# Kernel tuning notes

Hardware: AMD Instinct MI355X
Metric: run time of the kernel (lower is better)

## Reference

```python
import jax, jax.numpy as jnp
import numpy as np

N_NODES = 100000
N_EDGES = 1600000
IN_DIM = 64
HID_DIM = 32


def setup_inputs() -> dict:
    key = jax.random.key(0)
    k1, k2, k3, k4 = jax.random.split(key, 4)
    features = jax.random.normal(k1, (N_NODES, IN_DIM), dtype=jnp.float32)
    src = jax.random.randint(k2, (N_EDGES,), 0, N_NODES, dtype=jnp.int32)
    dst = jax.random.randint(k3, (N_EDGES,), 0, N_NODES, dtype=jnp.int32)
    # Glorot-uniform weight as in DGL GraphConv reset_parameters
    limit = (6.0 / (IN_DIM + HID_DIM)) ** 0.5
    W = jax.random.uniform(k4, (IN_DIM, HID_DIM), dtype=jnp.float32,
                           minval=-limit, maxval=limit)
    b = jnp.zeros((HID_DIM,), dtype=jnp.float32)
    return {"features": features, "src": src, "dst": dst, "W": W, "b": b}


def reference(features, src, dst, W, b):
    """DGL GraphConv(norm='both', activation=relu):
    out = relu(D_in^{-1/2} A D_out^{-1/2} (X W) + b)
    (weight applied first since in_dim > out_dim)."""
    n = features.shape[0]
    ones = jnp.ones(src.shape[0], dtype=features.dtype)
    deg_out = jax.ops.segment_sum(ones, src, num_segments=n)  # out-degree
    deg_in = jax.ops.segment_sum(ones, dst, num_segments=n)   # in-degree
    norm_src = jnp.clip(deg_out, 1.0, None) ** -0.5          # [N]
    norm_dst = jnp.clip(deg_in, 1.0, None) ** -0.5           # [N]

    h = (features @ W) * norm_src[:, None]                    # [N, hid]
    msg = h[src]                                              # [E, hid] gather
    agg = jax.ops.segment_sum(msg, dst, num_segments=n)       # [N, hid] scatter-add
    out = agg * norm_dst[:, None] + b
    return jax.nn.relu(out)
```

## Files before the change

### kernel.cpp

```cpp
#include <hip/hip_runtime.h>
#include <hip/hip_fp16.h>

#define IN_DIM 64
#define HID 32
#define SHIFT 8
#define BKEYS 256
#define CAP 4608
#define HCAP 2560
#define CHUNK 4096
#define MAXB 512

__global__ void zero_kernel(unsigned* __restrict__ p) {
    p[threadIdx.x + blockIdx.x * 256] = 0u;
}

__global__ __launch_bounds__(512) void multisplit_kernel(
    const int* __restrict__ src, const int* __restrict__ dst, int E, int NB,
    unsigned* __restrict__ gcur_d, unsigned* __restrict__ gcur_s,
    unsigned* __restrict__ bkt_pairs, unsigned char* __restrict__ bkt_srcs)
{
    __shared__ unsigned hist_d[MAXB], cur_d[MAXB], gb_d[MAXB];
    __shared__ unsigned hist_s[MAXB], cur_s[MAXB], gb_s[MAXB];
    int t = threadIdx.x;
    int e0 = blockIdx.x * CHUNK;
    int cnt = min(CHUNK, E - e0);
    hist_d[t] = 0; hist_s[t] = 0; cur_d[t] = 0; cur_s[t] = 0;
    __syncthreads();
    int n4 = cnt >> 2;
    const int4* s4 = (const int4*)(src + e0);
    const int4* d4 = (const int4*)(dst + e0);
    int4 sa = make_int4(-1, -1, -1, -1), da = sa, sb = sa, db = sa;
    if (t < n4)       { sa = s4[t];       da = d4[t]; }
    if (t + 512 < n4) { sb = s4[t + 512]; db = d4[t + 512]; }
    int sc = -1, dc = -1;
    int ti = (n4 << 2) + t;
    if (t < (cnt & 3)) { sc = src[e0 + ti]; dc = dst[e0 + ti]; }
    if (da.x >= 0) { atomicAdd(&hist_d[da.x >> SHIFT], 1u); atomicAdd(&hist_s[sa.x >> SHIFT], 1u);
                     atomicAdd(&hist_d[da.y >> SHIFT], 1u); atomicAdd(&hist_s[sa.y >> SHIFT], 1u);
                     atomicAdd(&hist_d[da.z >> SHIFT], 1u); atomicAdd(&hist_s[sa.z >> SHIFT], 1u);
                     atomicAdd(&hist_d[da.w >> SHIFT], 1u); atomicAdd(&hist_s[sa.w >> SHIFT], 1u); }
    if (db.x >= 0) { atomicAdd(&hist_d[db.x >> SHIFT], 1u); atomicAdd(&hist_s[sb.x >> SHIFT], 1u);
                     atomicAdd(&hist_d[db.y >> SHIFT], 1u); atomicAdd(&hist_s[sb.y >> SHIFT], 1u);
                     atomicAdd(&hist_d[db.z >> SHIFT], 1u); atomicAdd(&hist_s[sb.z >> SHIFT], 1u);
                     atomicAdd(&hist_d[db.w >> SHIFT], 1u); atomicAdd(&hist_s[sb.w >> SHIFT], 1u); }
    if (dc >= 0)   { atomicAdd(&hist_d[dc >> SHIFT], 1u);   atomicAdd(&hist_s[sc >> SHIFT], 1u); }
    __syncthreads();
    if (t < NB) {
        unsigned hd = hist_d[t], hs = hist_s[t];
        if (hd) gb_d[t] = atomicAdd(&gcur_d[t], hd);
        if (hs) gb_s[t] = atomicAdd(&gcur_s[t], hs);
    }
    __syncthreads();
    int dv[9] = {da.x, da.y, da.z, da.w, db.x, db.y, db.z, db.w, dc};
    int sv[9] = {sa.x, sa.y, sa.z, sa.w, sb.x, sb.y, sb.z, sb.w, sc};
#pragma unroll
    for (int j = 0; j < 9; ++j) {
        if (dv[j] < 0) continue;
        int kd = dv[j] >> SHIFT;
        unsigned pos = gb_d[kd] + atomicAdd(&cur_d[kd], 1u);
        if (pos < CAP)
            bkt_pairs[(size_t)kd * CAP + pos] =
                (((unsigned)dv[j] & (BKEYS - 1)) << 17) | (unsigned)sv[j];
        int ks = sv[j] >> SHIFT;
        unsigned pos2 = gb_s[ks] + atomicAdd(&cur_s[ks], 1u);
        if (pos2 < CAP)
            bkt_srcs[(size_t)ks * CAP + pos2] = (unsigned char)(sv[j] & (BKEYS - 1));
    }
}

__global__ __launch_bounds__(512) void degxw_kernel(
    const unsigned char* __restrict__ bkt_srcs, const unsigned* __restrict__ gcur_s,
    const float* __restrict__ X, const float* __restrict__ W,
    int N, unsigned short* __restrict__ h16)
{
    __shared__ float Ws[IN_DIM * HID];
    __shared__ unsigned cnt[128];
    __shared__ float nrm[128];
    int t = threadIdx.x;
    int blk = blockIdx.x, bin = blk >> 1;
    unsigned half = blk & 1;
    ((float4*)Ws)[t] = ((const float4*)W)[t];
    if (t < 128) cnt[t] = 0;
    __syncthreads();
    unsigned m = gcur_s[bin];
    if (m > CAP) m = CAP;
    const unsigned char* bs = bkt_srcs + (size_t)bin * CAP;
    const uchar4* bs4 = (const uchar4*)bs;
    unsigned m4 = m >> 2;
    for (unsigned i = t; i < m4; i += 512) {
        uchar4 kk = bs4[i];
        if ((kk.x >> 7) == half) atomicAdd(&cnt[kk.x & 127], 1u);
        if ((kk.y >> 7) == half) atomicAdd(&cnt[kk.y & 127], 1u);
        if ((kk.z >> 7) == half) atomicAdd(&cnt[kk.z & 127], 1u);
        if ((kk.w >> 7) == half) atomicAdd(&cnt[kk.w & 127], 1u);
    }
    for (unsigned i = (m4 << 2) + t; i < m; i += 512) {
        unsigned k = bs[i];
        if ((k >> 7) == half) atomicAdd(&cnt[k & 127], 1u);
    }
    __syncthreads();
    if (t < 128) nrm[t] = rsqrtf(fmaxf((float)cnt[t], 1.0f));
    __syncthreads();
    int q = t & 7, ln = t >> 3;
#pragma unroll
    for (int pass = 0; pass < 2; ++pass) {
        int lv = pass * 64 + ln;
        int v = bin * BKEYS + (int)half * 128 + lv;
        if (v < N) {
            const float4* Xr = (const float4*)(X + (size_t)v * IN_DIM);
            float4 acc = make_float4(0.f, 0.f, 0.f, 0.f);
#pragma unroll
            for (int kk = 0; kk < 16; ++kk) {
                float4 xv = Xr[kk];
                int k0 = kk * 4;
                float4 w0 = ((float4*)Ws)[(k0 + 0) * 8 + q];
                float4 w1 = ((float4*)Ws)[(k0 + 1) * 8 + q];
                float4 w2 = ((float4*)Ws)[(k0 + 2) * 8 + q];
                float4 w3 = ((float4*)Ws)[(k0 + 3) * 8 + q];
                acc.x += xv.x * w0.x + xv.y * w1.x + xv.z * w2.x + xv.w * w3.x;
                acc.y += xv.x * w0.y + xv.y * w1.y + xv.z * w2.y + xv.w * w3.y;
                acc.z += xv.x * w0.z + xv.y * w1.z + xv.z * w2.z + xv.w * w3.z;
                acc.w += xv.x * w0.w + xv.y * w1.w + xv.z * w2.w + xv.w * w3.w;
            }
            float s = nrm[lv];
            __half2 a  = __floats2half2_rn(acc.x * s, acc.y * s);
            __half2 b2 = __floats2half2_rn(acc.z * s, acc.w * s);
            uint2 u;
            u.x = *(unsigned*)&a;
            u.y = *(unsigned*)&b2;
            ((uint2*)h16)[(size_t)v * 8 + q] = u;
        }
    }
}

__global__ __launch_bounds__(512) void csrgather_kernel(
    const unsigned* __restrict__ bkt_pairs, const unsigned* __restrict__ gcur_d,
    const unsigned short* __restrict__ h16, const float* __restrict__ bias,
    float* __restrict__ out, int N)
{
    __shared__ unsigned cnt[128], ex[128], cur[128];
    __shared__ unsigned ecsr[HCAP];
    int t = threadIdx.x;
    int blk = blockIdx.x, bin = blk >> 1;
    unsigned half = blk & 1;
    if (t < 128) { cnt[t] = 0; cur[t] = 0; }
    __syncthreads();
    unsigned m = gcur_d[bin];
    if (m > CAP) m = CAP;
    const unsigned* bp = bkt_pairs + (size_t)bin * CAP;
    for (unsigned i = t; i < m; i += 512) {
        unsigned k = bp[i] >> 17;
        if ((k >> 7) == half) atomicAdd(&cnt[k & 127], 1u);
    }
    __syncthreads();
    if (t < 128) ex[t] = cnt[t];
    __syncthreads();
    for (int off = 1; off < 128; off <<= 1) {
        unsigned u = (t >= off && t < 128) ? ex[t - off] : 0;
        __syncthreads();
        if (t < 128) ex[t] += u;
        __syncthreads();
    }
    for (unsigned i = t; i < m; i += 512) {
        unsigned p = bp[i];
        unsigned k = p >> 17;
        if ((k >> 7) == half) {
            unsigned kk = k & 127;
            unsigned pos = (ex[kk] - cnt[kk]) + atomicAdd(&cur[kk], 1u);
            if (pos < HCAP) ecsr[pos] = p & 0x1FFFFu;
        }
    }
    __syncthreads();
    int lane = t & 63, w = t >> 6;
    int n16 = lane >> 2;
    int q = lane & 3;
    int lv = w * 16 + n16;
    unsigned dg = cnt[lv];
    unsigned en = ex[lv]; if (en > HCAP) en = HCAP;
    unsigned st = ex[lv] - dg; if (st > en) st = en;
    unsigned len = en - st;
    const uint4* h16q = (const uint4*)h16;

    float a0=0.f,a1=0.f,a2=0.f,a3=0.f,a4=0.f,a5=0.f,a6=0.f,a7=0.f;
    unsigned i = 0;
    for (; i + 4 <= len; i += 4) {
        unsigned s0 = ecsr[st + i];
        unsigned s1 = ecsr[st + i + 1];
        unsigned s2 = ecsr[st + i + 2];
        unsigned s3 = ecsr[st + i + 3];
        uint4 h0 = h16q[(size_t)s0 * 4 + q];
        uint4 h1 = h16q[(size_t)s1 * 4 + q];
        uint4 h2 = h16q[(size_t)s2 * 4 + q];
        uint4 h3 = h16q[(size_t)s3 * 4 + q];
        __half2* p0 = (__half2*)&h0;  __half2* p1 = (__half2*)&h1;
        __half2* p2 = (__half2*)&h2;  __half2* p3 = (__half2*)&h3;
        float2 f;
        f = __half22float2(p0[0]); a0 += f.x; a1 += f.y;
        f = __half22float2(p0[1]); a2 += f.x; a3 += f.y;
        f = __half22float2(p0[2]); a4 += f.x; a5 += f.y;
        f = __half22float2(p0[3]); a6 += f.x; a7 += f.y;
        f = __half22float2(p1[0]); a0 += f.x; a1 += f.y;
        f = __half22float2(p1[1]); a2 += f.x; a3 += f.y;
        f = __half22float2(p1[2]); a4 += f.x; a5 += f.y;
        f = __half22float2(p1[3]); a6 += f.x; a7 += f.y;
        f = __half22float2(p2[0]); a0 += f.x; a1 += f.y;
        f = __half22float2(p2[1]); a2 += f.x; a3 += f.y;
        f = __half22float2(p2[2]); a4 += f.x; a5 += f.y;
        f = __half22float2(p2[3]); a6 += f.x; a7 += f.y;
        f = __half22float2(p3[0]); a0 += f.x; a1 += f.y;
        f = __half22float2(p3[1]); a2 += f.x; a3 += f.y;
        f = __half22float2(p3[2]); a4 += f.x; a5 += f.y;
        f = __half22float2(p3[3]); a6 += f.x; a7 += f.y;
    }
    for (; i < len; ++i) {
        unsigned s = ecsr[st + i];
        uint4 hv = h16q[(size_t)s * 4 + q];
        __half2* hp = (__half2*)&hv;
        float2 f;
        f = __half22float2(hp[0]); a0 += f.x; a1 += f.y;
        f = __half22float2(hp[1]); a2 += f.x; a3 += f.y;
        f = __half22float2(hp[2]); a4 += f.x; a5 += f.y;
        f = __half22float2(hp[3]); a6 += f.x; a7 += f.y;
    }
    int v = bin * BKEYS + (int)half * 128 + lv;
    if (v < N) {
        float nv = rsqrtf(fmaxf((float)dg, 1.0f));
        float4 bq0 = ((const float4*)bias)[q * 2];
        float4 bq1 = ((const float4*)bias)[q * 2 + 1];
        float4 o0, o1;
        o0.x = fmaxf(a0 * nv + bq0.x, 0.f);
        o0.y = fmaxf(a1 * nv + bq0.y, 0.f);
        o0.z = fmaxf(a2 * nv + bq0.z, 0.f);
        o0.w = fmaxf(a3 * nv + bq0.w, 0.f);
        o1.x = fmaxf(a4 * nv + bq1.x, 0.f);
        o1.y = fmaxf(a5 * nv + bq1.y, 0.f);
        o1.z = fmaxf(a6 * nv + bq1.z, 0.f);
        o1.w = fmaxf(a7 * nv + bq1.w, 0.f);
        float* op = out + (size_t)v * HID + q * 8;
        *(float4*)op = o0;
        *(float4*)(op + 4) = o1;
    }
}

extern "C" void kernel_launch(void* const* d_in, const int* in_sizes, int n_in,
                              void* d_out, int out_size, void* d_ws, size_t ws_size,
                              hipStream_t stream) {
    const float* X   = (const float*)d_in[0];
    const int*   src = (const int*)d_in[1];
    const int*   dst = (const int*)d_in[2];
    const float* W   = (const float*)d_in[3];
    const float* b   = (const float*)d_in[4];
    float* out = (float*)d_out;

    int N = in_sizes[0] / IN_DIM;
    int E = in_sizes[1];
    int NB = (N + BKEYS - 1) / BKEYS;

    unsigned* gcur_d = (unsigned*)d_ws;
    unsigned* gcur_s = gcur_d + MAXB;
    unsigned* bkt_pairs = gcur_s + MAXB;
    unsigned char* bkt_srcs = (unsigned char*)(bkt_pairs + (size_t)NB * CAP);
    unsigned short* h16 = (unsigned short*)(bkt_srcs + (size_t)NB * CAP);

    zero_kernel<<<4, 256, 0, stream>>>(gcur_d);
    multisplit_kernel<<<(E + CHUNK - 1) / CHUNK, 512, 0, stream>>>(
        src, dst, E, NB, gcur_d, gcur_s, bkt_pairs, bkt_srcs);
    degxw_kernel<<<NB * 2, 512, 0, stream>>>(bkt_srcs, gcur_s, X, W, N, h16);
    csrgather_kernel<<<NB * 2, 512, 0, stream>>>(bkt_pairs, gcur_d, h16, b, out, N);
}
```

Baseline: 145.9 us.

## Split fp16 hidden features into two column planes to shrink gather working set

The fp16 projected features are stored as two separate 16-column planes instead of one interleaved 32-column row. The gather kernel now launches twice as many 256-thread blocks, each handling one plane, so each block gathers 32-byte rows from a half-size table. The intent is better cache locality for the random source-row gathers, since each plane's table fits more easily in L2/MALL. The cost is that every block rebuilds the bucket CSR in shared memory, so the edge-bucket scan and scatter work is doubled.

New measurement: 155.7 us. 1.07x slower.

```diff
diff --git a/kernel.cpp b/kernel.cpp
--- a/kernel.cpp
+++ b/kernel.cpp
@@ -102,6 +102,8 @@
     if (t < 128) nrm[t] = rsqrtf(fmaxf((float)cnt[t], 1.0f));
     __syncthreads();
     int q = t & 7, ln = t >> 3;
+    int plane = q >> 2, jq = q & 3;
+    uint2* hp = (uint2*)h16 + (size_t)plane * N * 4;
 #pragma unroll
     for (int pass = 0; pass < 2; ++pass) {
         int lv = pass * 64 + ln;
@@ -128,27 +130,30 @@
             uint2 u;
             u.x = *(unsigned*)&a;
             u.y = *(unsigned*)&b2;
-            ((uint2*)h16)[(size_t)v * 8 + q] = u;
+            hp[(size_t)v * 4 + jq] = u;
         }
     }
 }
 
-__global__ __launch_bounds__(512) void csrgather_kernel(
+__global__ __launch_bounds__(256) void csrgather_kernel(
     const unsigned* __restrict__ bkt_pairs, const unsigned* __restrict__ gcur_d,
     const unsigned short* __restrict__ h16, const float* __restrict__ bias,
-    float* __restrict__ out, int N)
+    float* __restrict__ out, int N, int NB)
 {
     __shared__ unsigned cnt[128], ex[128], cur[128];
     __shared__ unsigned ecsr[HCAP];
     int t = threadIdx.x;
-    int blk = blockIdx.x, bin = blk >> 1;
-    unsigned half = blk & 1;
+    int blk = blockIdx.x;
+    int plane = (blk >= 2 * NB) ? 1 : 0;
+    int blk2 = blk - plane * 2 * NB;
+    int bin = blk2 >> 1;
+    unsigned half = blk2 & 1;
     if (t < 128) { cnt[t] = 0; cur[t] = 0; }
     __syncthreads();
     unsigned m = gcur_d[bin];
     if (m > CAP) m = CAP;
     const unsigned* bp = bkt_pairs + (size_t)bin * CAP;
-    for (unsigned i = t; i < m; i += 512) {
+    for (unsigned i = t; i < m; i += 256) {
         unsigned k = bp[i] >> 17;
         if ((k >> 7) == half) atomicAdd(&cnt[k & 127], 1u);
     }
@@ -161,7 +166,7 @@
         if (t < 128) ex[t] += u;
         __syncthreads();
     }
-    for (unsigned i = t; i < m; i += 512) {
+    for (unsigned i = t; i < m; i += 256) {
         unsigned p = bp[i];
         unsigned k = p >> 17;
         if ((k >> 7) == half) {
@@ -172,14 +177,14 @@
     }
     __syncthreads();
     int lane = t & 63, w = t >> 6;
-    int n16 = lane >> 2;
-    int q = lane & 3;
-    int lv = w * 16 + n16;
+    int n32 = lane >> 1;
+    int j = lane & 1;
+    int lv = w * 32 + n32;
     unsigned dg = cnt[lv];
     unsigned en = ex[lv]; if (en > HCAP) en = HCAP;
     unsigned st = ex[lv] - dg; if (st > en) st = en;
     unsigned len = en - st;
-    const uint4* h16q = (const uint4*)h16;
+    const uint4* hq = (const uint4*)h16 + (size_t)plane * N * 2;
 
     float a0=0.f,a1=0.f,a2=0.f,a3=0.f,a4=0.f,a5=0.f,a6=0.f,a7=0.f;
     unsigned i = 0;
@@ -188,10 +193,10 @@
         unsigned s1 = ecsr[st + i + 1];
         unsigned s2 = ecsr[st + i + 2];
         unsigned s3 = ecsr[st + i + 3];
-        uint4 h0 = h16q[(size_t)s0 * 4 + q];
-        uint4 h1 = h16q[(size_t)s1 * 4 + q];
-        uint4 h2 = h16q[(size_t)s2 * 4 + q];
-        uint4 h3 = h16q[(size_t)s3 * 4 + q];
+        uint4 h0 = hq[(size_t)s0 * 2 + j];
+        uint4 h1 = hq[(size_t)s1 * 2 + j];
+        uint4 h2 = hq[(size_t)s2 * 2 + j];
+        uint4 h3 = hq[(size_t)s3 * 2 + j];
         __half2* p0 = (__half2*)&h0;  __half2* p1 = (__half2*)&h1;
         __half2* p2 = (__half2*)&h2;  __half2* p3 = (__half2*)&h3;
         float2 f;
@@ -214,7 +219,7 @@
     }
     for (; i < len; ++i) {
         unsigned s = ecsr[st + i];
-        uint4 hv = h16q[(size_t)s * 4 + q];
+        uint4 hv = hq[(size_t)s * 2 + j];
         __half2* hp = (__half2*)&hv;
         float2 f;
         f = __half22float2(hp[0]); a0 += f.x; a1 += f.y;
@@ -225,8 +230,8 @@
     int v = bin * BKEYS + (int)half * 128 + lv;
     if (v < N) {
         float nv = rsqrtf(fmaxf((float)dg, 1.0f));
-        float4 bq0 = ((const float4*)bias)[q * 2];
-        float4 bq1 = ((const float4*)bias)[q * 2 + 1];
+        float4 bq0 = ((const float4*)bias)[plane * 4 + j * 2];
+        float4 bq1 = ((const float4*)bias)[plane * 4 + j * 2 + 1];
         float4 o0, o1;
         o0.x = fmaxf(a0 * nv + bq0.x, 0.f);
         o0.y = fmaxf(a1 * nv + bq0.y, 0.f);
@@ -236,7 +241,7 @@
         o1.y = fmaxf(a5 * nv + bq1.y, 0.f);
         o1.z = fmaxf(a6 * nv + bq1.z, 0.f);
         o1.w = fmaxf(a7 * nv + bq1.w, 0.f);
-        float* op = out + (size_t)v * HID + q * 8;
+        float* op = out + (size_t)v * HID + plane * 16 + j * 8;
         *(float4*)op = o0;
         *(float4*)(op + 4) = o1;
     }
@@ -266,5 +271,5 @@
     multisplit_kernel<<<(E + CHUNK - 1) / CHUNK, 512, 0, stream>>>(
         src, dst, E, NB, gcur_d, gcur_s, bkt_pairs, bkt_srcs);
     degxw_kernel<<<NB * 2, 512, 0, stream>>>(bkt_srcs, gcur_s, X, W, N, h16);
-    csrgather_kernel<<<NB * 2, 512, 0, stream>>>(bkt_pairs, gcur_d, h16, b, out, N);
-}
+    csrgather_kernel<<<NB * 4, 256, 0, stream>>>(bkt_pairs, gcur_d, h16, b, out, N, NB);
+}
```
